# Kernel optimization log

Measured on AMD Instinct MI355X. Metric: run time of the kernel, lower is better.

## Reference

```python
import jax, jax.numpy as jnp
import numpy as np

B, N, C = 8, 1024, 768
H = 12
D = C // H            # 64
HID = int(C * 4.0)    # 3072
SCALE = D ** -0.5
EPS_LN = 1e-5
EPS_BN = 1e-5


def _layernorm(x, g, b):
    mu = jnp.mean(x, axis=-1, keepdims=True)
    var = jnp.mean(jnp.square(x - mu), axis=-1, keepdims=True)
    return (x - mu) * jax.lax.rsqrt(var + EPS_LN) * g + b


def setup_inputs() -> dict:
    key = jax.random.key(0)
    ks = jax.random.split(key, 12)
    s = lambda fan: 1.0 / np.sqrt(fan)
    inp = {
        "inputs": jax.random.normal(ks[0], (B, N, C), jnp.float32),
        "ln1_g": jnp.ones((C,), jnp.float32),
        "ln1_b": jnp.zeros((C,), jnp.float32),
        # nn.Linear(dim, 3*dim, bias=False)
        "qkv_w": jax.random.uniform(ks[1], (3 * C, C), jnp.float32, -s(C), s(C)),
        # nn.Conv2d(H, H, 1, 1) head-mixing matrix
        "conv_w": jax.random.uniform(ks[2], (H, H), jnp.float32, -s(H), s(H)),
        "conv_b": jax.random.uniform(ks[3], (H,), jnp.float32, -s(H), s(H)),
        # BatchNorm2d(H) in eval mode: affine params + running stats
        "bn_g": jnp.ones((H,), jnp.float32),
        "bn_b": jnp.zeros((H,), jnp.float32),
        "bn_rm": jnp.zeros((H,), jnp.float32),
        "bn_rv": jnp.ones((H,), jnp.float32),
        "proj_w": jax.random.uniform(ks[4], (C, C), jnp.float32, -s(C), s(C)),
        "proj_b": jax.random.uniform(ks[5], (C,), jnp.float32, -s(C), s(C)),
        "ln2_g": jnp.ones((C,), jnp.float32),
        "ln2_b": jnp.zeros((C,), jnp.float32),
        "fc1_w": jax.random.uniform(ks[6], (HID, C), jnp.float32, -s(C), s(C)),
        "fc1_b": jax.random.uniform(ks[7], (HID,), jnp.float32, -s(C), s(C)),
        "fc2_w": jax.random.uniform(ks[8], (C, HID), jnp.float32, -s(HID), s(HID)),
        "fc2_b": jax.random.uniform(ks[9], (C,), jnp.float32, -s(HID), s(HID)),
    }
    return inp


def reference(inputs, ln1_g, ln1_b, qkv_w, conv_w, conv_b, bn_g, bn_b, bn_rm, bn_rv,
              proj_w, proj_b, ln2_g, ln2_b, fc1_w, fc1_b, fc2_w, fc2_b):
    # adjust_ratio = 1.0, dropouts are identity (inference), BN uses running stats (eval)
    x_ln = _layernorm(inputs, ln1_g, ln1_b)
    qkv = (x_ln @ qkv_w.T).reshape(B, N, 3, H, D).transpose(2, 0, 3, 1, 4)
    q, k, v = qkv[0], qkv[1], qkv[2]
    attn = jax.nn.softmax(jnp.einsum('bhnd,bhmd->bhnm', q, k) * SCALE, axis=-1)
    # 1x1 conv across heads then BatchNorm2d (eval) * reatten_scale(=1.0)
    attn = jnp.einsum('oh,bhnm->bonm', conv_w, attn) + conv_b[None, :, None, None]
    bn_scale = bn_g * jax.lax.rsqrt(bn_rv + EPS_BN)
    attn = (attn - bn_rm[None, :, None, None]) * bn_scale[None, :, None, None] \
        + bn_b[None, :, None, None]
    attn_next = attn
    out = jnp.einsum('bhnm,bhmd->bhnd', attn, v).transpose(0, 2, 1, 3).reshape(B, N, C)
    out = out @ proj_w.T + proj_b
    x = inputs + out
    h = _layernorm(x, ln2_g, ln2_b)
    h = jax.nn.gelu(h @ fc1_w.T + fc1_b, approximate=False)
    x = x + (h @ fc2_w.T + fc2_b)
    return (x, attn_next)
```

## Files before the change

kernel.cpp:

```cpp
#include <hip/hip_runtime.h>
#include <cmath>

#define B_   8
#define N_   1024
#define C_   768
#define H_   12
#define D_   64
#define HID_ 3072
#define M_   8192

using frag  = __attribute__((ext_vector_type(8))) short;
using f32x4 = __attribute__((ext_vector_type(4))) float;
using s4v   = __attribute__((ext_vector_type(4))) short;

__device__ __forceinline__ short f2bf(float x) {
    union { float f; unsigned u; } v; v.f = x;
    unsigned r = (v.u + 0x7FFFu + ((v.u >> 16) & 1u)) >> 16;
    return (short)r;
}
__device__ __forceinline__ float gelu_exact(float x) {
    return 0.5f * x * (1.0f + erff(x * 0.70710678118654752f));
}
__device__ __forceinline__ void gload16(const void* g, void* l) {
    __builtin_amdgcn_global_load_lds(
        (const __attribute__((address_space(1))) void*)g,
        (__attribute__((address_space(3))) void*)l, 16, 0, 0);
}

__device__ __forceinline__ int2 swz_xy() {
    const int gx = gridDim.x;
    const int nwg = gx * gridDim.y;
    const int orig = blockIdx.y * gx + blockIdx.x;
    const int q = nwg >> 3, r = nwg & 7;
    const int xcd = orig & 7;
    const int base = (xcd < r) ? xcd * (q + 1) : r * (q + 1) + (xcd - r) * q;
    const int wgid = base + (orig >> 3);
    int2 v; v.x = wgid % gx; v.y = wgid / gx;
    return v;
}

#define NW0 (3 * C_ * C_)
#define NW1 (C_ * C_)
#define NW2 (HID_ * C_)
#define NW3 (C_ * HID_)
__global__ __launch_bounds__(256)
void cvt_weights(const float* __restrict__ s0, const float* __restrict__ s1,
                 const float* __restrict__ s2, const float* __restrict__ s3,
                 short* __restrict__ dst)
{
    long i = ((long)blockIdx.x * 256 + threadIdx.x) * 4;
    const float* s; long off;
    if      (i < NW0)             { s = s0; off = i; }
    else if (i < NW0 + NW1)       { s = s1; off = i - NW0; }
    else if (i < NW0 + NW1 + NW2) { s = s2; off = i - NW0 - NW1; }
    else                          { s = s3; off = i - NW0 - NW1 - NW2; }
    float4 u = *(const float4*)(s + off);
    s4v o; o[0] = f2bf(u.x); o[1] = f2bf(u.y); o[2] = f2bf(u.z); o[3] = f2bf(u.w);
    *(s4v*)(dst + i) = o;
}

__global__ __launch_bounds__(256)
void ln_bf16(const float* __restrict__ x, const float* __restrict__ g,
             const float* __restrict__ b, short* __restrict__ y)
{
    __shared__ float red[256];
    const long row = blockIdx.x;
    const float* xr = x + row * C_;
    short* yr = y + row * C_;
    const int t = threadIdx.x;
    float v0 = xr[t], v1 = xr[t + 256], v2 = xr[t + 512];
    red[t] = v0 + v1 + v2;
    __syncthreads();
    for (int o = 128; o > 0; o >>= 1) { if (t < o) red[t] += red[t + o]; __syncthreads(); }
    const float mu = red[0] * (1.0f / 768.0f);
    __syncthreads();
    const float d0 = v0 - mu, d1 = v1 - mu, d2 = v2 - mu;
    red[t] = d0 * d0 + d1 * d1 + d2 * d2;
    __syncthreads();
    for (int o = 128; o > 0; o >>= 1) { if (t < o) red[t] += red[t + o]; __syncthreads(); }
    const float rstd = rsqrtf(red[0] * (1.0f / 768.0f) + 1e-5f);
    yr[t]       = f2bf(d0 * rstd * g[t]       + b[t]);
    yr[t + 256] = f2bf(d1 * rstd * g[t + 256] + b[t + 256]);
    yr[t + 512] = f2bf(d2 * rstd * g[t + 512] + b[t + 512]);
}

template<int BM, int BN, int WGM, int WGN, bool AF32S, bool OUTF32,
         bool ACT_GELU, bool STATS, bool CW, bool NTC, int GMODE>
__global__ __launch_bounds__(256)
void gemm_mfma(const void* __restrict__ Ap, const float* __restrict__ Ap2,
               int lda, long sAb, long sAh,
               const short* __restrict__ Bp, int ldb, long sBb, long sBh,
               const float* __restrict__ bias,
               const float* __restrict__ res, int ldres,
               void* __restrict__ Cp, int ldc, long sCb, long sCh,
               float2* __restrict__ st,
               int K, float alpha)
{
    constexpr int FM = BM / (WGM * 16), FN = BN / (WGN * 16);
    __shared__ short As[BM * 64];
    __shared__ short Bs[BN * 64];
    const int tid = threadIdx.x;
    const int wid = tid >> 6, lane = tid & 63;
    int bx, by, z;
    if constexpr (GMODE == 1) {
        const int nwg = gridDim.x;
        const int qc = nwg >> 3;
        const int wg = (blockIdx.x & 7) * qc + (blockIdx.x >> 3);
        bx = 0; by = wg & 7; z = wg >> 3;
    } else {
        int2 v = swz_xy(); bx = v.x; by = v.y; z = blockIdx.z;
    }
    const int zb = z / H_, zh = z - zb * H_;
    const long m0 = (long)by * BM;
    const int  n0 = bx * BN;
    const short* Bb = Bp + zb * sBb + zh * sBh + (long)n0 * ldb;
    const short* Abh = nullptr; const float* Af0 = nullptr; const float* Af1 = nullptr;
    if constexpr (AF32S) { Af0 = (const float*)Ap + m0 * lda; Af1 = Ap2 + m0 * lda; }
    else                 Abh = (const short*)Ap + zb * sAb + zh * sAh + m0 * lda;
    f32x4 acc[FM][FN] = {};
    const int wr = wid / WGN, wc = wid - wr * WGN;
    const int srow = lane >> 3;
    const int schunk = (lane & 7) ^ srow;

    for (int k0 = 0; k0 < K; k0 += 64) {
        if constexpr (!AF32S) {
            for (int g = wid; g < BM / 8; g += 4)
                gload16(Abh + (long)(g * 8 + srow) * lda + k0 + schunk * 8, &As[g * 512]);
        } else {
            const int r = tid >> 1, h2 = tid & 1;
            const float* sp0 = Af0 + (long)r * lda + k0 + h2 * 32;
            const float* sp1 = Af1 + (long)r * lda + k0 + h2 * 32;
            #pragma unroll
            for (int j = 0; j < 4; ++j) {
                f32x4 a0 = *(const f32x4*)(sp0 + j * 8);
                f32x4 a1 = *(const f32x4*)(sp0 + j * 8 + 4);
                f32x4 b0 = *(const f32x4*)(sp1 + j * 8);
                f32x4 b1 = *(const f32x4*)(sp1 + j * 8 + 4);
                frag w;
                #pragma unroll
                for (int e = 0; e < 4; ++e) { w[e] = f2bf(a0[e] + b0[e]); w[e + 4] = f2bf(a1[e] + b1[e]); }
                *(frag*)&As[r * 64 + ((h2 * 4 + j) ^ (r & 7)) * 8] = w;
            }
        }
        for (int g = wid; g < BN / 8; g += 4)
            gload16(Bb + (long)(g * 8 + srow) * ldb + k0 + schunk * 8, &Bs[g * 512]);
        __syncthreads();
        #pragma unroll
        for (int kk = 0; kk < 2; ++kk) {
            frag a[FM], b[FN];
            #pragma unroll
            for (int fm = 0; fm < FM; ++fm) {
                const int r = wr * FM * 16 + fm * 16 + (lane & 15);
                const int ph = (kk * 4 + (lane >> 4)) ^ (r & 7);
                a[fm] = *(const frag*)&As[r * 64 + ph * 8];
            }
            #pragma unroll
            for (int fn = 0; fn < FN; ++fn) {
                const int r = wc * FN * 16 + fn * 16 + (lane & 15);
                const int ph = (kk * 4 + (lane >> 4)) ^ (r & 7);
                b[fn] = *(const frag*)&Bs[r * 64 + ph * 8];
            }
            #pragma unroll
            for (int fm = 0; fm < FM; ++fm)
                #pragma unroll
                for (int fn = 0; fn < FN; ++fn)
                    acc[fm][fn] = __builtin_amdgcn_mfma_f32_16x16x32_bf16(a[fm], b[fn], acc[fm][fn], 0, 0, 0);
        }
        __syncthreads();
    }

    if constexpr (CW) {
        float* Cf = (float*)Cp; short* Cs = (short*)Cp;
        const long cbase = zb * sCb + zh * sCh;
        #pragma unroll
        for (int fm = 0; fm < FM; ++fm) {
            #pragma unroll
            for (int fn = 0; fn < FN; ++fn) {
                const long rg = m0 + wr * FM * 16 + fm * 16 + ((lane >> 4) * 4);
                const int  cg = n0 + wc * FN * 16 + fn * 16 + (lane & 15);
                const float bv = bias ? bias[cg] : 0.0f;
                #pragma unroll
                for (int q = 0; q < 4; ++q) {
                    const long row = rg + q;
                    float v = acc[fm][fn][q] * alpha + bv;
                    if (res) v += res[row * (long)ldres + cg];
                    if constexpr (ACT_GELU) v = gelu_exact(v);
                    if constexpr (OUTF32) {
                        if constexpr (NTC) __builtin_nontemporal_store(v, &Cf[cbase + row * ldc + cg]);
                        else               Cf[cbase + row * ldc + cg] = v;
                    } else {
                        Cs[cbase + row * ldc + cg] = f2bf(v);
                    }
                }
            }
        }
    }

    if constexpr (STATS) {
        float* sred = (float*)As;
        float tmax[FM][4];
        #pragma unroll
        for (int fm = 0; fm < FM; ++fm)
            #pragma unroll
            for (int q = 0; q < 4; ++q) {
                float v = acc[fm][0][q];
                #pragma unroll
                for (int fn = 1; fn < FN; ++fn) v = fmaxf(v, acc[fm][fn][q]);
                v *= alpha;
                v = fmaxf(v, __shfl_xor(v, 1));
                v = fmaxf(v, __shfl_xor(v, 2));
                v = fmaxf(v, __shfl_xor(v, 4));
                v = fmaxf(v, __shfl_xor(v, 8));
                const int r = wr * FM * 16 + fm * 16 + (lane >> 4) * 4 + q;
                if ((lane & 15) == 0) sred[wc * BM + r] = v;
            }
        __syncthreads();
        #pragma unroll
        for (int fm = 0; fm < FM; ++fm)
            #pragma unroll
            for (int q = 0; q < 4; ++q) {
                const int r = wr * FM * 16 + fm * 16 + (lane >> 4) * 4 + q;
                tmax[fm][q] = fmaxf(sred[r], sred[BM + r]);
            }
        __syncthreads();
        #pragma unroll
        for (int fm = 0; fm < FM; ++fm)
            #pragma unroll
            for (int q = 0; q < 4; ++q) {
                float e = 0.0f;
                #pragma unroll
                for (int fn = 0; fn < FN; ++fn)
                    e += __expf(acc[fm][fn][q] * alpha - tmax[fm][q]);
                e += __shfl_xor(e, 1);
                e += __shfl_xor(e, 2);
                e += __shfl_xor(e, 4);
                e += __shfl_xor(e, 8);
                const int r = wr * FM * 16 + fm * 16 + (lane >> 4) * 4 + q;
                if ((lane & 15) == 0) sred[wc * BM + r] = e;
            }
        __syncthreads();
        if (wc == 0) {
            #pragma unroll
            for (int fm = 0; fm < FM; ++fm)
                #pragma unroll
                for (int q = 0; q < 4; ++q) {
                    const int r = wr * FM * 16 + fm * 16 + (lane >> 4) * 4 + q;
                    if ((lane & 15) == 0) {
                        float2 o; o.x = tmax[fm][q]; o.y = sred[r] + sred[BM + r];
                        st[((long)z * N_ + m0 + r) * 8 + bx] = o;
                    }
                }
        }
    }
}

__global__ __launch_bounds__(256)
void qksmpv(const short* __restrict__ qkvb, const short* __restrict__ vT,
            const float2* __restrict__ st,
            float* __restrict__ attn, float* __restrict__ Opart,
            const float* __restrict__ cw, const float* __restrict__ cb,
            const float* __restrict__ bg, const float* __restrict__ bb,
            const float* __restrict__ brm, const float* __restrict__ brv)
{
    __shared__ short qs[H_ * 16 * 64];
    __shared__ short ring[2][64 * 64];
    __shared__ short pm[4 * 16 * 64];
    __shared__ float smx[H_][16], sinv[H_][16];
    __shared__ float coef[H_][H_], baseA[H_], scA[H_];
    const int tid = threadIdx.x, wid = tid >> 6, lane = tid & 63;

    const int wg = (blockIdx.x & 7) * 128 + (blockIdx.x >> 3);
    const int b = wg >> 7, rem = wg & 127;
    const int nblk = rem >> 1, mhalf = rem & 1;
    const int n0 = nblk * 16, mbase = mhalf * 512;

    if (tid < H_) {
        const float s = bg[tid] * rsqrtf(brv[tid] + 1e-5f);
        scA[tid] = s;
        baseA[tid] = (cb[tid] - brm[tid]) * s + bb[tid];
    }
    __syncthreads();
    if (tid < H_ * H_) coef[tid / H_][tid % H_] = cw[tid] * scA[tid / H_];
    if (tid < 192) {
        const int h = tid >> 4, r = tid & 15;
        const float2* sp = st + ((long)(b * H_ + h) * N_ + n0 + r) * 8;
        float2 sv[8];
        #pragma unroll
        for (int i = 0; i < 8; ++i) sv[i] = sp[i];
        float gm = sv[0].x;
        #pragma unroll
        for (int i = 1; i < 8; ++i) gm = fmaxf(gm, sv[i].x);
        float gs = 0.0f;
        #pragma unroll
        for (int i = 0; i < 8; ++i) gs += sv[i].y * __expf(sv[i].x - gm);
        smx[h][r] = gm;
        sinv[h][r] = 1.0f / gs;
    }
    __syncthreads();

    const int srow = lane >> 3, schunk = (lane & 7) ^ srow;
    const short* qbase = qkvb + (long)(b * N_ + n0) * (3 * C_);
    for (int g = wid; g < 24; g += 4) {
        const int fr = g * 8 + srow;
        gload16(qbase + (long)(fr & 15) * (3 * C_) + (fr >> 4) * 64 + schunk * 8,
                &qs[g * 512]);
    }
    const short* kcol = qkvb + C_;
    {
        const short* kb = kcol + (long)(b * N_ + mbase) * (3 * C_);
        for (int g = wid; g < 8; g += 4)
            gload16(kb + (long)(g * 8 + srow) * (3 * C_) + schunk * 8, &ring[0][g * 512]);
    }

    f32x4 oacc[H_] = {};
    const int rowb = (lane >> 4) * 4;
    const int colw = wid * 16 + (lane & 15);
    const long vbb = (long)b * H_ * (D_ * N_);
    int t = 0;

    for (int mc = 0; mc < 8; ++mc) {
        const int mo = mbase + mc * 64;
        const short* kb = kcol + (long)(b * N_ + mo) * (3 * C_);
        float macc[H_][4] = {};

        #pragma unroll 1
        for (int h = 0; h < H_; ++h) {
            asm volatile("s_waitcnt vmcnt(0)" ::: "memory");
            __builtin_amdgcn_sched_barrier(0);
            __builtin_amdgcn_s_barrier();
            if (h < H_ - 1) {
                for (int g = wid; g < 8; g += 4)
                    gload16(kb + (long)(g * 8 + srow) * (3 * C_) + (h + 1) * 64 + schunk * 8,
                            &ring[(t + 1) & 1][g * 512]);
            } else {
                const short* vb = vT + vbb + mo;
                for (int g = wid; g < 8; g += 4)
                    gload16(vb + (long)(g * 8 + srow) * N_ + schunk * 8,
                            &ring[(t + 1) & 1][g * 512]);
            }
            f32x4 acc = {};
            const int afr = h * 16 + (lane & 15);
            #pragma unroll
            for (int kk = 0; kk < 2; ++kk) {
                const frag a  = *(const frag*)&qs[afr * 64 + (((kk * 4 + (lane >> 4)) ^ (afr & 7))) * 8];
                const frag bv = *(const frag*)&ring[t & 1][colw * 64 + (((kk * 4 + (lane >> 4)) ^ (colw & 7))) * 8];
                acc = __builtin_amdgcn_mfma_f32_16x16x32_bf16(a, bv, acc, 0, 0, 0);
            }
            #pragma unroll
            for (int q = 0; q < 4; ++q) {
                const float e = __expf(acc[q] * 0.125f - smx[h][rowb + q]) * sinv[h][rowb + q];
                #pragma unroll
                for (int o = 0; o < H_; ++o) macc[o][q] += coef[o][h] * e;
            }
            ++t;
        }

        #pragma unroll
        for (int o = 0; o < H_; ++o) {
            float* ap = attn + ((long)(b * H_ + o) << 20) + ((long)(n0 + rowb) << 10) + mo + colw;
            #pragma unroll
            for (int q = 0; q < 4; ++q)
                __builtin_nontemporal_store(macc[o][q] + baseA[o], ap + ((long)q << 10));
        }

        #pragma unroll
        for (int pass = 0; pass < 3; ++pass) {
            asm volatile("s_waitcnt lgkmcnt(0)" ::: "memory");
            __builtin_amdgcn_sched_barrier(0);
            __builtin_amdgcn_s_barrier();
            #pragma unroll
            for (int ol = 0; ol < 4; ++ol) {
                const int o = pass * 4 + ol;
                #pragma unroll
                for (int q = 0; q < 4; ++q) {
                    const int row = ol * 16 + rowb + q;
                    const int ch = (colw >> 3) ^ (row & 7);
                    pm[row * 64 + ch * 8 + (colw & 7)] = f2bf(macc[o][q] + baseA[o]);
                }
            }
            #pragma unroll
            for (int ov = 0; ov < 4; ++ov) {
                const int o = pass * 4 + ov;
                asm volatile("s_waitcnt vmcnt(0) lgkmcnt(0)" ::: "memory");
                __builtin_amdgcn_sched_barrier(0);
                __builtin_amdgcn_s_barrier();
                if (o < H_ - 1) {
                    const short* vb = vT + vbb + (long)(o + 1) * (D_ * N_) + mo;
                    for (int g = wid; g < 8; g += 4)
                        gload16(vb + (long)(g * 8 + srow) * N_ + schunk * 8,
                                &ring[(t + 1) & 1][g * 512]);
                } else if (mc < 7) {
                    const short* kb2 = kcol + (long)(b * N_ + mbase + (mc + 1) * 64) * (3 * C_);
                    for (int g = wid; g < 8; g += 4)
                        gload16(kb2 + (long)(g * 8 + srow) * (3 * C_) + schunk * 8,
                                &ring[(t + 1) & 1][g * 512]);
                }
                #pragma unroll
                for (int kk = 0; kk < 2; ++kk) {
                    const int ar = ov * 16 + (lane & 15);
                    const frag a  = *(const frag*)&pm[ar * 64 + (((kk * 4 + (lane >> 4)) ^ (ar & 7))) * 8];
                    const int br = wid * 16 + (lane & 15);
                    const frag bv = *(const frag*)&ring[t & 1][br * 64 + (((kk * 4 + (lane >> 4)) ^ (br & 7))) * 8];
                    oacc[o] = __builtin_amdgcn_mfma_f32_16x16x32_bf16(a, bv, oacc[o], 0, 0, 0);
                }
                ++t;
            }
        }
    }

    float* op = Opart + (long)mhalf * M_ * C_;
    #pragma unroll
    for (int o = 0; o < H_; ++o) {
        #pragma unroll
        for (int q = 0; q < 4; ++q)
            op[(long)(b * N_ + n0 + rowb + q) * C_ + o * D_ + wid * 16 + (lane & 15)] = oacc[o][q];
    }
}

__global__ __launch_bounds__(256)
void vtrans(const short* __restrict__ qkv, short* __restrict__ vT)
{
    __shared__ short tile[64][72];
    const int bh = blockIdx.x;
    const int n0 = blockIdx.y * 64;
    const int b = bh / H_, h = bh - b * H_;
    const short* src = qkv + (long)b * N_ * (3 * C_) + 2 * C_ + h * D_;
    const int t = threadIdx.x;
    {
        const int r = t >> 2, c = (t & 3) * 16;
        const short* sp = src + (long)(n0 + r) * (3 * C_) + c;
        #pragma unroll
        for (int j = 0; j < 16; j++) tile[r][c + j] = sp[j];
    }
    __syncthreads();
    {
        const int d = t >> 2, c = (t & 3) * 16;
        short* dp = vT + (long)bh * (D_ * N_) + (long)d * N_ + n0 + c;
        #pragma unroll
        for (int j = 0; j < 16; j++) dp[j] = tile[c + j][d];
    }
}

extern "C" void kernel_launch(void* const* d_in, const int* in_sizes, int n_in,
                              void* d_out, int out_size, void* d_ws, size_t ws_size,
                              hipStream_t stream)
{
    const float* inp    = (const float*)d_in[0];
    const float* ln1_g  = (const float*)d_in[1];
    const float* ln1_b  = (const float*)d_in[2];
    const float* qkv_w  = (const float*)d_in[3];
    const float* conv_w = (const float*)d_in[4];
    const float* conv_b = (const float*)d_in[5];
    const float* bn_g   = (const float*)d_in[6];
    const float* bn_b   = (const float*)d_in[7];
    const float* bn_rm  = (const float*)d_in[8];
    const float* bn_rv  = (const float*)d_in[9];
    const float* proj_w = (const float*)d_in[10];
    const float* proj_b = (const float*)d_in[11];
    const float* ln2_g  = (const float*)d_in[12];
    const float* ln2_b  = (const float*)d_in[13];
    const float* fc1_w  = (const float*)d_in[14];
    const float* fc1_b  = (const float*)d_in[15];
    const float* fc2_w  = (const float*)d_in[16];
    const float* fc2_b  = (const float*)d_in[17];

    float* outx = (float*)d_out;
    float* attn = outx + (long)M_ * C_;

    char* w = (char*)d_ws;
    short* wqkv  = (short*)w;  w += (long)NW0 * 2;
    short* wproj = (short*)w;  w += (long)NW1 * 2;
    short* wfc1  = (short*)w;  w += (long)NW2 * 2;
    short* wfc2  = (short*)w;  w += (long)NW3 * 2;
    short* xln   = (short*)w;  w += (long)M_ * C_ * 2;
    short* qkvb  = (short*)w;
    short* hbuf  = qkvb;       w += (long)M_ * HID_ * 2;
    short* vT    = (short*)w;  w += (long)B_ * H_ * D_ * N_ * 2;
    float* xres  = (float*)w;  w += (long)M_ * C_ * 4;
    float2* st   = (float2*)w; w += (long)B_ * H_ * N_ * 8 * 8;
    float* Opart = (float*)w;  w += (long)2 * M_ * C_ * 4;

    cvt_weights<<<(NW0 + NW1 + NW2 + NW3) / 1024, 256, 0, stream>>>(
        qkv_w, proj_w, fc1_w, fc2_w, wqkv);

    ln_bf16<<<M_, 256, 0, stream>>>(inp, ln1_g, ln1_b, xln);

    gemm_mfma<128, 128, 2, 2, false, false, false, false, true, false, 0>
        <<<dim3(18, 64, 1), 256, 0, stream>>>(
        xln, nullptr, C_, 0, 0, wqkv, C_, 0, 0, nullptr, nullptr, 0,
        qkvb, 3 * C_, 0, 0, nullptr, C_, 1.0f);

    vtrans<<<dim3(B_ * H_, 16), 256, 0, stream>>>(qkvb, vT);

    gemm_mfma<128, 128, 2, 2, false, false, false, true, false, false, 0>
        <<<dim3(8, 8, 96), 256, 0, stream>>>(
        qkvb, nullptr, 3 * C_, (long)N_ * 3 * C_, D_,
        qkvb + C_,     3 * C_, (long)N_ * 3 * C_, D_,
        nullptr, nullptr, 0,
        nullptr, N_, 0, 0, st, D_, 0.125f);

    qksmpv<<<1024, 256, 0, stream>>>(qkvb, vT, st, attn, Opart,
                                     conv_w, conv_b, bn_g, bn_b, bn_rm, bn_rv);

    gemm_mfma<128, 64, 4, 1, true, true, false, false, true, false, 0>
        <<<dim3(12, 64, 1), 256, 0, stream>>>(
        Opart, Opart + (long)M_ * C_, C_, 0, 0,
        wproj, C_, 0, 0, proj_b, inp, C_,
        xres, C_, 0, 0, nullptr, C_, 1.0f);

    ln_bf16<<<M_, 256, 0, stream>>>(xres, ln2_g, ln2_b, xln);

    gemm_mfma<128, 128, 2, 2, false, false, true, false, true, false, 0>
        <<<dim3(24, 64, 1), 256, 0, stream>>>(
        xln, nullptr, C_, 0, 0, wfc1, C_, 0, 0, fc1_b, nullptr, 0,
        hbuf, HID_, 0, 0, nullptr, C_, 1.0f);

    gemm_mfma<128, 64, 4, 1, false, true, false, false, true, true, 0>
        <<<dim3(12, 64, 1), 256, 0, stream>>>(
        hbuf, nullptr, HID_, 0, 0, wfc2, HID_, 0, 0, fc2_b, xres, C_,
        outx, C_, 0, 0, nullptr, HID_, 1.0f);
}
```

Measured before the change: 623.6 us.

## Hold Q fragments in registers and triple-buffer K/V staging ring

The fused attention kernel now loads each block's Q tile straight into registers instead of staging it in shared memory. The K/V ring grows from two to three buffers, and a unified stage schedule keeps two loads in flight, waiting with vmcnt(2) instead of vmcnt(0). The pm write barrier is also restructured so it sits after the prefetch is issued. This is meant to hide global load latency behind MFMA and exp work. The cost is many more registers (24 frags of Q plus the 48-float macc), which risks lower occupancy or spills.

```diff
diff --git a/kernel.cpp b/kernel.cpp
--- a/kernel.cpp
+++ b/kernel.cpp
@@ -262,8 +262,7 @@
             const float* __restrict__ bg, const float* __restrict__ bb,
             const float* __restrict__ brm, const float* __restrict__ brv)
 {
-    __shared__ short qs[H_ * 16 * 64];
-    __shared__ short ring[2][64 * 64];
+    __shared__ short ring[3][64 * 64];
     __shared__ short pm[4 * 16 * 64];
     __shared__ float smx[H_][16], sinv[H_][16];
     __shared__ float coef[H_][H_], baseA[H_], scA[H_];
@@ -298,53 +297,63 @@
     }
     __syncthreads();
 
+    frag qreg[H_][2];
+    {
+        const short* qrow = qkvb + (long)(b * N_ + n0 + (lane & 15)) * (3 * C_)
+                          + (lane >> 4) * 8;
+        #pragma unroll
+        for (int h = 0; h < H_; ++h)
+            #pragma unroll
+            for (int kk = 0; kk < 2; ++kk)
+                qreg[h][kk] = *(const frag*)(qrow + h * 64 + kk * 32);
+    }
+
     const int srow = lane >> 3, schunk = (lane & 7) ^ srow;
-    const short* qbase = qkvb + (long)(b * N_ + n0) * (3 * C_);
-    for (int g = wid; g < 24; g += 4) {
-        const int fr = g * 8 + srow;
-        gload16(qbase + (long)(fr & 15) * (3 * C_) + (fr >> 4) * 64 + schunk * 8,
-                &qs[g * 512]);
-    }
     const short* kcol = qkvb + C_;
-    {
-        const short* kb = kcol + (long)(b * N_ + mbase) * (3 * C_);
-        for (int g = wid; g < 8; g += 4)
-            gload16(kb + (long)(g * 8 + srow) * (3 * C_) + schunk * 8, &ring[0][g * 512]);
-    }
+    const long vbb = (long)b * H_ * (D_ * N_);
+
+    auto stage = [&](int g) {
+        const int mcs = g / 24, js = g - mcs * 24;
+        const int mos = mbase + mcs * 64;
+        if (js < 12) {
+            const short* kb = kcol + (long)(b * N_ + mos) * (3 * C_) + js * 64;
+            for (int gg = wid; gg < 8; gg += 4)
+                gload16(kb + (long)(gg * 8 + srow) * (3 * C_) + schunk * 8,
+                        &ring[g % 3][gg * 512]);
+        } else {
+            const short* vb = vT + vbb + (long)(js - 12) * (D_ * N_) + mos;
+            for (int gg = wid; gg < 8; gg += 4)
+                gload16(vb + (long)(gg * 8 + srow) * N_ + schunk * 8,
+                        &ring[g % 3][gg * 512]);
+        }
+    };
+
+    stage(0);
+    stage(1);
 
     f32x4 oacc[H_] = {};
     const int rowb = (lane >> 4) * 4;
     const int colw = wid * 16 + (lane & 15);
-    const long vbb = (long)b * H_ * (D_ * N_);
-    int t = 0;
-
+
+    #pragma unroll 1
     for (int mc = 0; mc < 8; ++mc) {
         const int mo = mbase + mc * 64;
-        const short* kb = kcol + (long)(b * N_ + mo) * (3 * C_);
+        const int gbase = mc * 24;
         float macc[H_][4] = {};
 
-        #pragma unroll 1
+        #pragma unroll
         for (int h = 0; h < H_; ++h) {
-            asm volatile("s_waitcnt vmcnt(0)" ::: "memory");
+            const int g = gbase + h;
+            asm volatile("s_waitcnt vmcnt(2)" ::: "memory");
             __builtin_amdgcn_sched_barrier(0);
             __builtin_amdgcn_s_barrier();
-            if (h < H_ - 1) {
-                for (int g = wid; g < 8; g += 4)
-                    gload16(kb + (long)(g * 8 + srow) * (3 * C_) + (h + 1) * 64 + schunk * 8,
-                            &ring[(t + 1) & 1][g * 512]);
-            } else {
-                const short* vb = vT + vbb + mo;
-                for (int g = wid; g < 8; g += 4)
-                    gload16(vb + (long)(g * 8 + srow) * N_ + schunk * 8,
-                            &ring[(t + 1) & 1][g * 512]);
-            }
+            if (g + 2 < 192) stage(g + 2);
             f32x4 acc = {};
-            const int afr = h * 16 + (lane & 15);
             #pragma unroll
             for (int kk = 0; kk < 2; ++kk) {
-                const frag a  = *(const frag*)&qs[afr * 64 + (((kk * 4 + (lane >> 4)) ^ (afr & 7))) * 8];
-                const frag bv = *(const frag*)&ring[t & 1][colw * 64 + (((kk * 4 + (lane >> 4)) ^ (colw & 7))) * 8];
-                acc = __builtin_amdgcn_mfma_f32_16x16x32_bf16(a, bv, acc, 0, 0, 0);
+                const frag bv = *(const frag*)&ring[g % 3]
+                    [colw * 64 + (((kk * 4 + (lane >> 4)) ^ (colw & 7))) * 8];
+                acc = __builtin_amdgcn_mfma_f32_16x16x32_bf16(qreg[h][kk], bv, acc, 0, 0, 0);
             }
             #pragma unroll
             for (int q = 0; q < 4; ++q) {
@@ -352,7 +361,6 @@
                 #pragma unroll
                 for (int o = 0; o < H_; ++o) macc[o][q] += coef[o][h] * e;
             }
-            ++t;
         }
 
         #pragma unroll
@@ -365,45 +373,40 @@
 
         #pragma unroll
         for (int pass = 0; pass < 3; ++pass) {
-            asm volatile("s_waitcnt lgkmcnt(0)" ::: "memory");
-            __builtin_amdgcn_sched_barrier(0);
-            __builtin_amdgcn_s_barrier();
-            #pragma unroll
-            for (int ol = 0; ol < 4; ++ol) {
-                const int o = pass * 4 + ol;
-                #pragma unroll
-                for (int q = 0; q < 4; ++q) {
-                    const int row = ol * 16 + rowb + q;
-                    const int ch = (colw >> 3) ^ (row & 7);
-                    pm[row * 64 + ch * 8 + (colw & 7)] = f2bf(macc[o][q] + baseA[o]);
-                }
-            }
             #pragma unroll
             for (int ov = 0; ov < 4; ++ov) {
-                const int o = pass * 4 + ov;
-                asm volatile("s_waitcnt vmcnt(0) lgkmcnt(0)" ::: "memory");
+                const int g = gbase + 12 + pass * 4 + ov;
+                if (g == 191) asm volatile("s_waitcnt vmcnt(0)" ::: "memory");
+                else          asm volatile("s_waitcnt vmcnt(2)" ::: "memory");
                 __builtin_amdgcn_sched_barrier(0);
                 __builtin_amdgcn_s_barrier();
-                if (o < H_ - 1) {
-                    const short* vb = vT + vbb + (long)(o + 1) * (D_ * N_) + mo;
-                    for (int g = wid; g < 8; g += 4)
-                        gload16(vb + (long)(g * 8 + srow) * N_ + schunk * 8,
-                                &ring[(t + 1) & 1][g * 512]);
-                } else if (mc < 7) {
-                    const short* kb2 = kcol + (long)(b * N_ + mbase + (mc + 1) * 64) * (3 * C_);
-                    for (int g = wid; g < 8; g += 4)
-                        gload16(kb2 + (long)(g * 8 + srow) * (3 * C_) + schunk * 8,
-                                &ring[(t + 1) & 1][g * 512]);
+                if (g + 2 < 192) stage(g + 2);
+                if (ov == 0) {
+                    #pragma unroll
+                    for (int ol = 0; ol < 4; ++ol) {
+                        const int o = pass * 4 + ol;
+                        #pragma unroll
+                        for (int q = 0; q < 4; ++q) {
+                            const int row = ol * 16 + rowb + q;
+                            const int ch = (colw >> 3) ^ (row & 7);
+                            pm[row * 64 + ch * 8 + (colw & 7)] = f2bf(macc[o][q] + baseA[o]);
+                        }
+                    }
+                    asm volatile("s_waitcnt lgkmcnt(0)" ::: "memory");
+                    __builtin_amdgcn_sched_barrier(0);
+                    __builtin_amdgcn_s_barrier();
                 }
+                const int o = pass * 4 + ov;
                 #pragma unroll
                 for (int kk = 0; kk < 2; ++kk) {
                     const int ar = ov * 16 + (lane & 15);
-                    const frag a  = *(const frag*)&pm[ar * 64 + (((kk * 4 + (lane >> 4)) ^ (ar & 7))) * 8];
+                    const frag a  = *(const frag*)&pm
+                        [ar * 64 + (((kk * 4 + (lane >> 4)) ^ (ar & 7))) * 8];
                     const int br = wid * 16 + (lane & 15);
-                    const frag bv = *(const frag*)&ring[t & 1][br * 64 + (((kk * 4 + (lane >> 4)) ^ (br & 7))) * 8];
+                    const frag bv = *(const frag*)&ring[g % 3]
+                        [br * 64 + (((kk * 4 + (lane >> 4)) ^ (br & 7))) * 8];
                     oacc[o] = __builtin_amdgcn_mfma_f32_16x16x32_bf16(a, bv, oacc[o], 0, 0, 0);
                 }
-                ++t;
             }
         }
     }
```

Result: slower. 813.7 us (+30.5%).
